# Kernel tuning notes

Measured on AMD Instinct MI355X. Metric: run time of the kernel, lower is better.

The kernel has to match this reference:

```python
import jax, jax.numpy as jnp
import numpy as np
import math

B, C, H, W = 4, 256, 56, 56
RC = 32  # max(256 // 8, 8)
EPS = 1e-5


def _conv(x, w, pad):
    return jax.lax.conv_general_dilated(
        x, w, window_strides=(1, 1), padding=[(pad, pad), (pad, pad)],
        dimension_numbers=('NCHW', 'OIHW', 'NCHW'))


def setup_inputs() -> dict:
    key = jax.random.key(0)
    ks = jax.random.split(key, 9)
    s = 0.05  # keep attention logits in a sane range
    return {
        'x': jax.random.normal(ks[0], (B, C, H, W), jnp.float32),
        'wq1': jax.random.normal(ks[1], (RC, C, 1, 1), jnp.float32) * s,
        'wq3': jax.random.normal(ks[2], (RC, C, 3, 3), jnp.float32) * s,
        'wq5': jax.random.normal(ks[3], (RC, C, 5, 5), jnp.float32) * s,
        'wq7': jax.random.normal(ks[4], (RC, C, 7, 7), jnp.float32) * s,
        'wk': jax.random.normal(ks[5], (RC, C, 1, 1), jnp.float32) * s,
        'wv': jax.random.normal(ks[6], (C, C, 1, 1), jnp.float32) * s,
        'wproj': jax.random.normal(ks[7], (C, 4 * C, 1, 1), jnp.float32) * s,
        'gamma': jnp.ones((C,), jnp.float32),
        'beta': jnp.zeros((C,), jnp.float32),
    }


def reference(x, wq1, wq3, wq5, wq7, wk, wv, wproj, gamma, beta):
    b, c, h, w = x.shape
    hw = h * w
    scale = 1.0 / math.sqrt(RC)
    k = _conv(x, wk, 0).reshape(b, RC, hw)   # [B, RC, HW]
    v = _conv(x, wv, 0).reshape(b, c, hw)    # [B, C, HW]
    attended = []
    for wq, pad in ((wq1, 0), (wq3, 1), (wq5, 2), (wq7, 3)):
        q = _conv(x, wq, pad).reshape(b, RC, hw)          # [B, RC, HW]
        scores = jnp.einsum('bri,brj->bij', q, k) * scale  # [B, HW, HW]
        attn = jax.nn.softmax(scores, axis=-1)
        att = jnp.einsum('bcj,bij->bci', v, attn)          # [B, C, HW]
        attended.append(att.reshape(b, c, h, w))
    concat = jnp.concatenate(attended, axis=1)             # [B, 4C, H, W]
    out = _conv(concat, wproj, 0) + x                      # residual before BN
    # BatchNorm2d in training mode: batch stats (biased var), affine
    mean = out.mean(axis=(0, 2, 3), keepdims=True)
    var = out.var(axis=(0, 2, 3), keepdims=True)
    out = (out - mean) * jax.lax.rsqrt(var + EPS)
    return out * gamma[None, :, None, None] + beta[None, :, None, None]
```

## Files before the change

kernel.cpp:

```cpp
#include <hip/hip_runtime.h>
#include <hip/hip_bf16.h>
#include <math.h>

#define HW 3136
#define WIDTH 56
#define CC 256
#define BB 4
#define RCH 32
#define NJT (HW / 64)
#define TSPLIT 25
#define SCLOG2E 0.2550437041556575f

using bf16x8 = __attribute__((ext_vector_type(8))) short;
using f32x4  = __attribute__((ext_vector_type(4))) float;

static __device__ __forceinline__ unsigned short f2bf(float f) {
    __hip_bfloat16 h = __float2bfloat16(f);
    return *reinterpret_cast<unsigned short*>(&h);
}

__global__ __launch_bounds__(256) void prep_weights(
    const float* __restrict__ wq3, const float* __restrict__ wq5,
    const float* __restrict__ wq7, const float* __restrict__ wproj,
    const float* __restrict__ wk, const float* __restrict__ wq1,
    const float* __restrict__ wv,
    unsigned short* __restrict__ Wb3, unsigned short* __restrict__ Wb5,
    unsigned short* __restrict__ Wb7, unsigned short* __restrict__ Wpb,
    unsigned short* __restrict__ Wkq, unsigned short* __restrict__ Wvb) {
    int e = blockIdx.x * 256 + threadIdx.x;
    if (e < 73728) {
        int c = e & 255, r = (e >> 8) & 31, t = e >> 13;
        Wb3[e] = f2bf(wq3[((size_t)r * 256 + c) * 9 + t]);
    } else if (e < 278528) {
        int i = e - 73728;
        int c = i & 255, r = (i >> 8) & 31, t = i >> 13;
        Wb5[i] = f2bf(wq5[((size_t)r * 256 + c) * 25 + t]);
    } else if (e < 679936) {
        int i = e - 278528;
        int c = i & 255, r = (i >> 8) & 31, t = i >> 13;
        Wb7[i] = f2bf(wq7[((size_t)r * 256 + c) * 49 + t]);
    } else if (e < 942080) {
        int i = e - 679936;
        Wpb[i] = f2bf(wproj[i]);
    } else if (e < 958464) {
        int i = e - 942080;
        Wkq[i] = f2bf(i < 8192 ? wk[i] : wq1[i - 8192]);
    } else if (e < 1024000) {
        int i = e - 958464;
        Wvb[i] = f2bf(wv[i]);
    }
}

__global__ __launch_bounds__(256) void transpose_x(
    const float* __restrict__ x, unsigned short* __restrict__ xT) {
    __shared__ unsigned short tile[32][33];
    const int b = blockIdx.z;
    const int i0 = blockIdx.x * 32, c0 = blockIdx.y * 32;
    const int tx = threadIdx.x & 31, ty = threadIdx.x >> 5;
    #pragma unroll
    for (int k = 0; k < 4; ++k)
        tile[ty + k * 8][tx] = f2bf(x[((size_t)b * CC + c0 + ty + k * 8) * HW + i0 + tx]);
    __syncthreads();
    #pragma unroll
    for (int k = 0; k < 4; ++k)
        xT[((size_t)b * HW + i0 + ty + k * 8) * 256 + c0 + tx] = tile[tx][ty + k * 8];
}

__global__ __launch_bounds__(256) void qk32_mfma(
    const unsigned short* __restrict__ xT, const unsigned short* __restrict__ Wkq,
    unsigned short* __restrict__ Kt, unsigned short* __restrict__ Qt) {
    const int b = blockIdx.y, z = blockIdx.z;
    const int i0 = blockIdx.x * 64;
    const int t = threadIdx.x;
    const int lane = t & 63, w = t >> 6, lg = lane >> 4, li = lane & 15;

    unsigned short* outp = z == 0 ? Kt : Qt;
    const float osc = z == 0 ? 1.0f : SCLOG2E;
    const unsigned short* wb = Wkq + z * 8192;
    const unsigned short* xb = xT + ((size_t)b * HW + i0 + w * 16 + li) * 256;

    const f32x4 z4 = (f32x4){0.f, 0.f, 0.f, 0.f};
    f32x4 acc[2] = {z4, z4};

    for (int c0 = 0; c0 < 256; c0 += 32) {
        bf16x8 ax = *(const bf16x8*)(xb + c0 + lg * 8);
        #pragma unroll
        for (int rs = 0; rs < 2; ++rs) {
            bf16x8 bw = *(const bf16x8*)(wb + (size_t)(rs * 16 + li) * 256 + c0 + lg * 8);
            acc[rs] = __builtin_amdgcn_mfma_f32_16x16x32_bf16(ax, bw, acc[rs], 0, 0, 0);
        }
    }
    unsigned short* qb = outp + ((size_t)b * HW + i0 + w * 16 + lg * 4) * 32;
    #pragma unroll
    for (int rs = 0; rs < 2; ++rs)
        #pragma unroll
        for (int r = 0; r < 4; ++r)
            qb[(size_t)r * 32 + rs * 16 + li] = f2bf(acc[rs][r] * osc);
}

__global__ __launch_bounds__(256) void v_mfma(
    const unsigned short* __restrict__ xT, const unsigned short* __restrict__ Wvb,
    unsigned short* __restrict__ Vb) {
    const int b = blockIdx.y;
    const int i0 = blockIdx.x * 32;
    const int t = threadIdx.x;
    const int lane = t & 63, w = t >> 6, lg = lane >> 4, li = lane & 15;

    const f32x4 z4 = (f32x4){0.f, 0.f, 0.f, 0.f};
    f32x4 acc[4][2];
    #pragma unroll
    for (int ct = 0; ct < 4; ++ct) { acc[ct][0] = z4; acc[ct][1] = z4; }

    const unsigned short* xb = xT + (size_t)b * HW * 256;

    for (int c0 = 0; c0 < 256; c0 += 32) {
        bf16x8 bx[2];
        #pragma unroll
        for (int is = 0; is < 2; ++is)
            bx[is] = *(const bf16x8*)(xb + (size_t)(i0 + is * 16 + li) * 256 + c0 + lg * 8);
        #pragma unroll
        for (int ct = 0; ct < 4; ++ct) {
            bf16x8 aw = *(const bf16x8*)(
                Wvb + (size_t)(w * 64 + ct * 16 + li) * 256 + c0 + lg * 8);
            #pragma unroll
            for (int is = 0; is < 2; ++is)
                acc[ct][is] = __builtin_amdgcn_mfma_f32_16x16x32_bf16(
                    aw, bx[is], acc[ct][is], 0, 0, 0);
        }
    }
    #pragma unroll
    for (int ct = 0; ct < 4; ++ct)
        #pragma unroll
        for (int is = 0; is < 2; ++is)
            #pragma unroll
            for (int r = 0; r < 4; ++r)
                Vb[((size_t)b * CC + w * 64 + ct * 16 + lg * 4 + r) * HW +
                   i0 + is * 16 + li] = f2bf(acc[ct][is][r]);
}

template <int KS>
static __device__ __forceinline__ void qconv_body(
    const unsigned short* __restrict__ xT,
    const unsigned short* __restrict__ Wb,
    unsigned short* __restrict__ q,
    unsigned short (*xs)[40]) {
    constexpr int P = (KS - 1) / 2;
    constexpr int KT = KS * KS;
    constexpr int ROWS = 64 + 114 * P;
    const int b = blockIdx.y;
    const int i0 = blockIdx.x * 64;
    const int t = threadIdx.x;
    const int lane = t & 63;
    const int w = t >> 6;
    const int li = lane & 15;
    const int lg = lane >> 4;

    const int base = i0 - P * 57;
    const int mycol = (i0 + w * 16 + li) % WIDTH;

    f32x4 acc[2];
    acc[0] = (f32x4){0.f, 0.f, 0.f, 0.f};
    acc[1] = (f32x4){0.f, 0.f, 0.f, 0.f};

    const unsigned short* xTb = xT + (size_t)b * HW * 256;

    for (int c0 = 0; c0 < 256; c0 += 32) {
        __syncthreads();
        for (int e = t; e < ROWS * 4; e += 256) {
            int row = e >> 2, cs = e & 3;
            int gidx = base + row;
            uint4 val = make_uint4(0, 0, 0, 0);
            if (gidx >= 0 && gidx < HW)
                val = *(const uint4*)(xTb + (size_t)gidx * 256 + c0 + cs * 8);
            *(uint4*)(&xs[row][cs * 8]) = val;
        }
        __syncthreads();

        #pragma unroll
        for (int tap = 0; tap < KT; ++tap) {
            const int dx = tap % KS - P;
            const int poff = (tap / KS) * WIDTH + tap % KS;
            bf16x8 a = *(const bf16x8*)(&xs[w * 16 + li + poff][lg * 8]);
            if ((unsigned)(mycol + dx) >= (unsigned)WIDTH)
                a = (bf16x8){0, 0, 0, 0, 0, 0, 0, 0};
            const unsigned short* wrow =
                Wb + (size_t)tap * 32 * 256 + c0 + lg * 8;
            bf16x8 b0 = *(const bf16x8*)(wrow + (size_t)li * 256);
            bf16x8 b1 = *(const bf16x8*)(wrow + (size_t)(16 + li) * 256);
            acc[0] = __builtin_amdgcn_mfma_f32_16x16x32_bf16(a, b0, acc[0], 0, 0, 0);
            acc[1] = __builtin_amdgcn_mfma_f32_16x16x32_bf16(a, b1, acc[1], 0, 0, 0);
        }
    }

    unsigned short* qb = q + ((size_t)b * HW + i0 + w * 16 + lg * 4) * 32;
    #pragma unroll
    for (int rs = 0; rs < 2; ++rs)
        #pragma unroll
        for (int r = 0; r < 4; ++r)
            qb[(size_t)r * 32 + rs * 16 + li] = f2bf(acc[rs][r] * SCLOG2E);
}

__global__ __launch_bounds__(256) void qconv_all(
    const unsigned short* __restrict__ xT,
    const unsigned short* __restrict__ Wb3,
    const unsigned short* __restrict__ Wb5,
    const unsigned short* __restrict__ Wb7,
    unsigned short* __restrict__ Qt) {
    __shared__ unsigned short xs[406][40];
    const size_t QSLICE = (size_t)BB * HW * 32;
    if (blockIdx.z == 0)      qconv_body<3>(xT, Wb3, Qt + 1 * QSLICE, xs);
    else if (blockIdx.z == 1) qconv_body<5>(xT, Wb5, Qt + 2 * QSLICE, xs);
    else                      qconv_body<7>(xT, Wb7, Qt + 3 * QSLICE, xs);
}

__global__ __launch_bounds__(256) void flashmfma(
    const unsigned short* __restrict__ Qt, const unsigned short* __restrict__ Kt,
    const unsigned short* __restrict__ Vb, unsigned short* __restrict__ P0,
    unsigned short* __restrict__ P1, float* __restrict__ Lsum) {
    const int F = blockIdx.x;
    const int xcd = F & 7;
    const int within = F >> 3;
    const int q4 = within / 49;
    const int i0 = (within % 49) * 64;
    const int pair = xcd + 8 * (q4 & 1);
    const int split = q4 >> 1;
    const int b = pair & 3;
    const int g = pair >> 2;

    const int t = threadIdx.x;
    const int lane = t & 63;
    const int w = t >> 6;
    const int lg = lane >> 4;
    const int li = lane & 15;

    __shared__ __align__(16) unsigned short Ps[64][72];

    const bf16x8 aq = *(const bf16x8*)(
        Qt + ((size_t)(g * BB + b) * HW + i0 + w * 16 + li) * 32 + lg * 8);

    const f32x4 z4 = (f32x4){0.f, 0.f, 0.f, 0.f};
    f32x4 acc[4][4];
    #pragma unroll
    for (int ct = 0; ct < 4; ++ct)
        #pragma unroll
        for (int is = 0; is < 4; ++is) acc[ct][is] = z4;

    float lsum[4] = {0.f, 0.f, 0.f, 0.f};

    const unsigned short* Kb = Kt + (size_t)b * HW * 32;
    const unsigned short* Vw = Vb + ((size_t)b * CC + w * 64) * HW;

    const int jt0 = split == 0 ? 0 : TSPLIT;
    const int jt1 = split == 0 ? TSPLIT : NJT;

    for (int jt = jt0; jt < jt1; ++jt) {
        const int j0 = jt * 64;

        bf16x8 vf[4][2];
        #pragma unroll
        for (int ct = 0; ct < 4; ++ct) {
            vf[ct][0] = *(const bf16x8*)(
                Vw + (size_t)(ct * 16 + li) * HW + j0 + lg * 8);
            vf[ct][1] = *(const bf16x8*)(
                Vw + (size_t)(ct * 16 + li) * HW + j0 + 32 + lg * 8);
        }

        f32x4 S[4];
        #pragma unroll
        for (int j2 = 0; j2 < 4; ++j2) {
            bf16x8 bk = *(const bf16x8*)(Kb + (size_t)(j0 + j2 * 16 + li) * 32 + lg * 8);
            S[j2] = __builtin_amdgcn_mfma_f32_16x16x32_bf16(aq, bk, z4, 0, 0, 0);
        }

        unsigned int pk0[4], pk1[4];
        #pragma unroll
        for (int r = 0; r < 4; ++r) {
            float p0 = __builtin_amdgcn_exp2f(S[0][r]);
            float p1 = __builtin_amdgcn_exp2f(S[1][r]);
            float p2 = __builtin_amdgcn_exp2f(S[2][r]);
            float p3 = __builtin_amdgcn_exp2f(S[3][r]);
            lsum[r] += (p0 + p1) + (p2 + p3);
            asm("v_cvt_pk_bf16_f32 %0, %1, %2" : "=v"(pk0[r]) : "v"(p0), "v"(p1));
            asm("v_cvt_pk_bf16_f32 %0, %1, %2" : "=v"(pk1[r]) : "v"(p2), "v"(p3));
        }

        __syncthreads();
        #pragma unroll
        for (int r = 0; r < 4; ++r) {
            const int row = w * 16 + lg * 4 + r;
            Ps[row][li]      = (unsigned short)pk0[r];
            Ps[row][16 + li] = (unsigned short)(pk0[r] >> 16);
            Ps[row][32 + li] = (unsigned short)pk1[r];
            Ps[row][48 + li] = (unsigned short)(pk1[r] >> 16);
        }
        __syncthreads();

        bf16x8 bp[4][2];
        #pragma unroll
        for (int is = 0; is < 4; ++is)
            #pragma unroll
            for (int ks = 0; ks < 2; ++ks)
                bp[is][ks] = *(const bf16x8*)(&Ps[is * 16 + li][ks * 32 + lg * 8]);

        __builtin_amdgcn_s_setprio(1);
        #pragma unroll
        for (int ct = 0; ct < 4; ++ct) {
            #pragma unroll
            for (int is = 0; is < 4; ++is) {
                acc[ct][is] = __builtin_amdgcn_mfma_f32_16x16x32_bf16(
                    vf[ct][0], bp[is][0], acc[ct][is], 0, 0, 0);
                acc[ct][is] = __builtin_amdgcn_mfma_f32_16x16x32_bf16(
                    vf[ct][1], bp[is][1], acc[ct][is], 0, 0, 0);
            }
        }
        __builtin_amdgcn_s_setprio(0);
    }

    #pragma unroll
    for (int r = 0; r < 4; ++r) {
        float s = lsum[r];
        #pragma unroll
        for (int off = 1; off < 16; off <<= 1) s += __shfl_xor(s, off);
        if (li == 0)
            Lsum[(size_t)split * 16 * HW + (size_t)(g * BB + b) * HW +
                 i0 + w * 16 + lg * 4 + r] = s;
    }

    unsigned short* Pp = split == 0 ? P0 : P1;
    #pragma unroll
    for (int ct = 0; ct < 4; ++ct)
        #pragma unroll
        for (int is = 0; is < 4; ++is) {
            unsigned int lo, hi;
            asm("v_cvt_pk_bf16_f32 %0, %1, %2"
                : "=v"(lo) : "v"(acc[ct][is][0]), "v"(acc[ct][is][1]));
            asm("v_cvt_pk_bf16_f32 %0, %1, %2"
                : "=v"(hi) : "v"(acc[ct][is][2]), "v"(acc[ct][is][3]));
            uint2 pk; pk.x = lo; pk.y = hi;
            *(uint2*)(Pp + ((size_t)b * HW + i0 + is * 16 + li) * 1024 +
                      g * 256 + w * 64 + ct * 16 + lg * 4) = pk;
        }
}

__global__ __launch_bounds__(256) void combine_att(
    unsigned short* __restrict__ Pio, const unsigned short* __restrict__ P1,
    const float* __restrict__ Lsum) {
    const int b = blockIdx.y;
    const int hw = blockIdx.x * 2 + (threadIdx.x >> 7);
    const int lp = threadIdx.x & 127;
    const int c0 = lp * 8;
    const int g = c0 >> 8;

    const size_t lidx = (size_t)(g * BB + b) * HW + hw;
    const float invl = 1.f / (Lsum[lidx] + Lsum[(size_t)16 * HW + lidx]);

    const size_t off = ((size_t)b * HW + hw) * 1024 + c0;
    uint4 ua = *(const uint4*)(Pio + off);
    uint4 ub = *(const uint4*)(P1 + off);
    unsigned int a[4] = {ua.x, ua.y, ua.z, ua.w};
    unsigned int bb[4] = {ub.x, ub.y, ub.z, ub.w};
    unsigned int o[4];
    #pragma unroll
    for (int k = 0; k < 4; ++k) {
        float a0 = __uint_as_float(a[k] << 16);
        float a1 = __uint_as_float(a[k] & 0xffff0000u);
        float b0 = __uint_as_float(bb[k] << 16);
        float b1 = __uint_as_float(bb[k] & 0xffff0000u);
        float f0 = (a0 + b0) * invl;
        float f1 = (a1 + b1) * invl;
        asm("v_cvt_pk_bf16_f32 %0, %1, %2" : "=v"(o[k]) : "v"(f0), "v"(f1));
    }
    uint4 uo; uo.x = o[0]; uo.y = o[1]; uo.z = o[2]; uo.w = o[3];
    *(uint4*)(Pio + off) = uo;
}

__global__ __launch_bounds__(256) void gemm_proj(
    const unsigned short* __restrict__ ATTt, const unsigned short* __restrict__ Wpb,
    const float* __restrict__ x, float* __restrict__ out) {
    const int b = blockIdx.y;
    const int i0 = blockIdx.x * 32;
    const int t = threadIdx.x;
    const int lane = t & 63;
    const int w = t >> 6;
    const int lg = lane >> 4;
    const int li = lane & 15;

    const f32x4 z4 = (f32x4){0.f, 0.f, 0.f, 0.f};
    f32x4 acc[4][2];
    #pragma unroll
    for (int ct = 0; ct < 4; ++ct) { acc[ct][0] = z4; acc[ct][1] = z4; }

    const unsigned short* ab = ATTt + (size_t)b * HW * 1024;

    for (int k0 = 0; k0 < 1024; k0 += 32) {
        bf16x8 afr[2];
        #pragma unroll
        for (int is = 0; is < 2; ++is)
            afr[is] = *(const bf16x8*)(
                ab + (size_t)(i0 + is * 16 + li) * 1024 + k0 + lg * 8);
        #pragma unroll
        for (int ct = 0; ct < 4; ++ct) {
            bf16x8 wf = *(const bf16x8*)(
                Wpb + (size_t)(w * 64 + ct * 16 + li) * 1024 + k0 + lg * 8);
            #pragma unroll
            for (int is = 0; is < 2; ++is)
                acc[ct][is] = __builtin_amdgcn_mfma_f32_16x16x32_bf16(
                    wf, afr[is], acc[ct][is], 0, 0, 0);
        }
    }

    #pragma unroll
    for (int ct = 0; ct < 4; ++ct)
        #pragma unroll
        for (int is = 0; is < 2; ++is)
            #pragma unroll
            for (int r = 0; r < 4; ++r) {
                int co = w * 64 + ct * 16 + lg * 4 + r;
                size_t o = ((size_t)b * CC + co) * HW + i0 + is * 16 + li;
                out[o] = acc[ct][is][r] + x[o];
            }
}

__global__ __launch_bounds__(256) void bnstats(
    const float* __restrict__ out, float* __restrict__ mean,
    float* __restrict__ rstd) {
    const int c = blockIdx.x;
    float s = 0.f, s2 = 0.f;
    for (int e = threadIdx.x; e < BB * HW; e += 256) {
        int b = e / HW, i = e - b * HW;
        float v = out[((size_t)b * CC + c) * HW + i];
        s += v; s2 += v * v;
    }
    __shared__ float rs[256], rs2[256];
    rs[threadIdx.x] = s; rs2[threadIdx.x] = s2;
    __syncthreads();
    for (int st = 128; st > 0; st >>= 1) {
        if (threadIdx.x < st) {
            rs[threadIdx.x] += rs[threadIdx.x + st];
            rs2[threadIdx.x] += rs2[threadIdx.x + st];
        }
        __syncthreads();
    }
    if (threadIdx.x == 0) {
        const float n = (float)(BB * HW);
        float m = rs[0] / n;
        float var = rs2[0] / n - m * m;
        mean[c] = m;
        rstd[c] = rsqrtf(var + 1e-5f);
    }
}

__global__ __launch_bounds__(256) void bnapply(
    float* __restrict__ out, const float* __restrict__ mean,
    const float* __restrict__ rstd, const float* __restrict__ gamma,
    const float* __restrict__ beta) {
    size_t idx = (size_t)blockIdx.x * 256 + threadIdx.x;
    if (idx < (size_t)BB * CC * HW) {
        int c = (int)((idx / HW) % CC);
        out[idx] = (out[idx] - mean[c]) * rstd[c] * gamma[c] + beta[c];
    }
}

extern "C" void kernel_launch(void* const* d_in, const int* in_sizes, int n_in,
                              void* d_out, int out_size, void* d_ws, size_t ws_size,
                              hipStream_t stream) {
    const float* x     = (const float*)d_in[0];
    const float* wq1   = (const float*)d_in[1];
    const float* wq3   = (const float*)d_in[2];
    const float* wq5   = (const float*)d_in[3];
    const float* wq7   = (const float*)d_in[4];
    const float* wk    = (const float*)d_in[5];
    const float* wv    = (const float*)d_in[6];
    const float* wproj = (const float*)d_in[7];
    const float* gamma = (const float*)d_in[8];
    const float* beta  = (const float*)d_in[9];
    float* out = (float*)d_out;

    unsigned short* P0   = (unsigned short*)d_ws;
    unsigned short* P1   = P0 + (size_t)BB * HW * 1024;
    float* Lsum          = (float*)(P1 + (size_t)BB * HW * 1024);
    unsigned short* Kt   = (unsigned short*)(Lsum + (size_t)2 * 16 * HW);
    unsigned short* Qt   = Kt + (size_t)BB * HW * 32;
    unsigned short* Vb   = Qt + (size_t)4 * BB * HW * 32;
    unsigned short* xT   = Vb + (size_t)BB * CC * HW;
    unsigned short* Wb3  = xT + (size_t)BB * HW * CC;
    unsigned short* Wb5  = Wb3 + (size_t)9 * 32 * 256;
    unsigned short* Wb7  = Wb5 + (size_t)25 * 32 * 256;
    unsigned short* Wpb  = Wb7 + (size_t)49 * 32 * 256;
    unsigned short* Wkq  = Wpb + (size_t)256 * 1024;
    unsigned short* Wvb  = Wkq + (size_t)2 * 32 * 256;
    float* mean = (float*)(Wvb + (size_t)256 * 256);
    float* rstd = mean + CC;

    dim3 blk(256);

    prep_weights<<<dim3(4000), blk, 0, stream>>>(
        wq3, wq5, wq7, wproj, wk, wq1, wv, Wb3, Wb5, Wb7, Wpb, Wkq, Wvb);
    transpose_x<<<dim3(HW / 32, CC / 32, BB), blk, 0, stream>>>(x, xT);

    qk32_mfma<<<dim3(HW / 64, BB, 2), blk, 0, stream>>>(xT, Wkq, Kt, Qt);
    v_mfma<<<dim3(HW / 32, BB), blk, 0, stream>>>(xT, Wvb, Vb);

    qconv_all<<<dim3(HW / 64, BB, 3), blk, 0, stream>>>(xT, Wb3, Wb5, Wb7, Qt);

    flashmfma<<<dim3(8 * 4 * (HW / 64)), blk, 0, stream>>>(Qt, Kt, Vb, P0, P1, Lsum);
    combine_att<<<dim3(HW / 2, BB), blk, 0, stream>>>(P0, P1, Lsum);

    gemm_proj<<<dim3(HW / 32, BB), blk, 0, stream>>>(P0, Wpb, x, out);

    bnstats<<<dim3(CC), blk, 0, stream>>>(out, mean, rstd);
    bnapply<<<dim3((BB * CC * HW + 255) / 256), blk, 0, stream>>>(out, mean, rstd, gamma, beta);
}
```

Before: 486.0 us.

## Fuse split-softmax combine into projection GEMM and merge 3x3/5x5 q-convs

Result: no change. 485.9 us (-0.0%).

```diff
diff --git a/kernel.cpp b/kernel.cpp
--- a/kernel.cpp
+++ b/kernel.cpp
@@ -200,6 +200,83 @@
             qb[(size_t)r * 32 + rs * 16 + li] = f2bf(acc[rs][r] * SCLOG2E);
 }
 
+static __device__ __forceinline__ void qconv35_body(
+    const unsigned short* __restrict__ xT,
+    const unsigned short* __restrict__ Wb3,
+    const unsigned short* __restrict__ Wb5,
+    unsigned short* __restrict__ q3, unsigned short* __restrict__ q5,
+    unsigned short (*xs)[40]) {
+    constexpr int P = 2;
+    constexpr int ROWS = 64 + 114 * P;
+    const int b = blockIdx.y;
+    const int i0 = blockIdx.x * 64;
+    const int t = threadIdx.x;
+    const int lane = t & 63;
+    const int w = t >> 6;
+    const int li = lane & 15;
+    const int lg = lane >> 4;
+
+    const int base = i0 - P * 57;
+    const int mycol = (i0 + w * 16 + li) % WIDTH;
+
+    const f32x4 z4 = (f32x4){0.f, 0.f, 0.f, 0.f};
+    f32x4 acc3[2] = {z4, z4}, acc5[2] = {z4, z4};
+
+    const unsigned short* xTb = xT + (size_t)b * HW * 256;
+
+    for (int c0 = 0; c0 < 256; c0 += 32) {
+        __syncthreads();
+        for (int e = t; e < ROWS * 4; e += 256) {
+            int row = e >> 2, cs = e & 3;
+            int gidx = base + row;
+            uint4 val = make_uint4(0, 0, 0, 0);
+            if (gidx >= 0 && gidx < HW)
+                val = *(const uint4*)(xTb + (size_t)gidx * 256 + c0 + cs * 8);
+            *(uint4*)(&xs[row][cs * 8]) = val;
+        }
+        __syncthreads();
+
+        #pragma unroll
+        for (int dy = -2; dy <= 2; ++dy) {
+            #pragma unroll
+            for (int dx = -2; dx <= 2; ++dx) {
+                const int poff = (dy + 2) * WIDTH + (dx + 2);
+                bf16x8 a = *(const bf16x8*)(&xs[w * 16 + li + poff][lg * 8]);
+                if ((unsigned)(mycol + dx) >= (unsigned)WIDTH)
+                    a = (bf16x8){0, 0, 0, 0, 0, 0, 0, 0};
+                {
+                    const int t5 = (dy + 2) * 5 + (dx + 2);
+                    const unsigned short* wrow =
+                        Wb5 + (size_t)t5 * 32 * 256 + c0 + lg * 8;
+                    bf16x8 b0 = *(const bf16x8*)(wrow + (size_t)li * 256);
+                    bf16x8 b1 = *(const bf16x8*)(wrow + (size_t)(16 + li) * 256);
+                    acc5[0] = __builtin_amdgcn_mfma_f32_16x16x32_bf16(a, b0, acc5[0], 0, 0, 0);
+                    acc5[1] = __builtin_amdgcn_mfma_f32_16x16x32_bf16(a, b1, acc5[1], 0, 0, 0);
+                }
+                if (dy >= -1 && dy <= 1 && dx >= -1 && dx <= 1) {
+                    const int t3 = (dy + 1) * 3 + (dx + 1);
+                    const unsigned short* wrow =
+                        Wb3 + (size_t)t3 * 32 * 256 + c0 + lg * 8;
+                    bf16x8 b0 = *(const bf16x8*)(wrow + (size_t)li * 256);
+                    bf16x8 b1 = *(const bf16x8*)(wrow + (size_t)(16 + li) * 256);
+                    acc3[0] = __builtin_amdgcn_mfma_f32_16x16x32_bf16(a, b0, acc3[0], 0, 0, 0);
+                    acc3[1] = __builtin_amdgcn_mfma_f32_16x16x32_bf16(a, b1, acc3[1], 0, 0, 0);
+                }
+            }
+        }
+    }
+
+    unsigned short* qb3 = q3 + ((size_t)b * HW + i0 + w * 16 + lg * 4) * 32;
+    unsigned short* qb5 = q5 + ((size_t)b * HW + i0 + w * 16 + lg * 4) * 32;
+    #pragma unroll
+    for (int rs = 0; rs < 2; ++rs)
+        #pragma unroll
+        for (int r = 0; r < 4; ++r) {
+            qb3[(size_t)r * 32 + rs * 16 + li] = f2bf(acc3[rs][r] * SCLOG2E);
+            qb5[(size_t)r * 32 + rs * 16 + li] = f2bf(acc5[rs][r] * SCLOG2E);
+        }
+}
+
 __global__ __launch_bounds__(256) void qconv_all(
     const unsigned short* __restrict__ xT,
     const unsigned short* __restrict__ Wb3,
@@ -208,9 +285,10 @@
     unsigned short* __restrict__ Qt) {
     __shared__ unsigned short xs[406][40];
     const size_t QSLICE = (size_t)BB * HW * 32;
-    if (blockIdx.z == 0)      qconv_body<3>(xT, Wb3, Qt + 1 * QSLICE, xs);
-    else if (blockIdx.z == 1) qconv_body<5>(xT, Wb5, Qt + 2 * QSLICE, xs);
-    else                      qconv_body<7>(xT, Wb7, Qt + 3 * QSLICE, xs);
+    if (blockIdx.z == 0)
+        qconv_body<7>(xT, Wb7, Qt + 3 * QSLICE, xs);
+    else
+        qconv35_body(xT, Wb3, Wb5, Qt + 1 * QSLICE, Qt + 2 * QSLICE, xs);
 }
 
 __global__ __launch_bounds__(256) void flashmfma(
@@ -342,40 +420,9 @@
         }
 }
 
-__global__ __launch_bounds__(256) void combine_att(
-    unsigned short* __restrict__ Pio, const unsigned short* __restrict__ P1,
-    const float* __restrict__ Lsum) {
-    const int b = blockIdx.y;
-    const int hw = blockIdx.x * 2 + (threadIdx.x >> 7);
-    const int lp = threadIdx.x & 127;
-    const int c0 = lp * 8;
-    const int g = c0 >> 8;
-
-    const size_t lidx = (size_t)(g * BB + b) * HW + hw;
-    const float invl = 1.f / (Lsum[lidx] + Lsum[(size_t)16 * HW + lidx]);
-
-    const size_t off = ((size_t)b * HW + hw) * 1024 + c0;
-    uint4 ua = *(const uint4*)(Pio + off);
-    uint4 ub = *(const uint4*)(P1 + off);
-    unsigned int a[4] = {ua.x, ua.y, ua.z, ua.w};
-    unsigned int bb[4] = {ub.x, ub.y, ub.z, ub.w};
-    unsigned int o[4];
-    #pragma unroll
-    for (int k = 0; k < 4; ++k) {
-        float a0 = __uint_as_float(a[k] << 16);
-        float a1 = __uint_as_float(a[k] & 0xffff0000u);
-        float b0 = __uint_as_float(bb[k] << 16);
-        float b1 = __uint_as_float(bb[k] & 0xffff0000u);
-        float f0 = (a0 + b0) * invl;
-        float f1 = (a1 + b1) * invl;
-        asm("v_cvt_pk_bf16_f32 %0, %1, %2" : "=v"(o[k]) : "v"(f0), "v"(f1));
-    }
-    uint4 uo; uo.x = o[0]; uo.y = o[1]; uo.z = o[2]; uo.w = o[3];
-    *(uint4*)(Pio + off) = uo;
-}
-
 __global__ __launch_bounds__(256) void gemm_proj(
-    const unsigned short* __restrict__ ATTt, const unsigned short* __restrict__ Wpb,
+    const unsigned short* __restrict__ P0, const unsigned short* __restrict__ P1,
+    const unsigned short* __restrict__ Wpb, const float* __restrict__ Lsum,
     const float* __restrict__ x, float* __restrict__ out) {
     const int b = blockIdx.y;
     const int i0 = blockIdx.x * 32;
@@ -386,27 +433,55 @@
     const int li = lane & 15;
 
     const f32x4 z4 = (f32x4){0.f, 0.f, 0.f, 0.f};
-    f32x4 acc[4][2];
-    #pragma unroll
-    for (int ct = 0; ct < 4; ++ct) { acc[ct][0] = z4; acc[ct][1] = z4; }
-
-    const unsigned short* ab = ATTt + (size_t)b * HW * 1024;
-
-    for (int k0 = 0; k0 < 1024; k0 += 32) {
-        bf16x8 afr[2];
-        #pragma unroll
-        for (int is = 0; is < 2; ++is)
-            afr[is] = *(const bf16x8*)(
-                ab + (size_t)(i0 + is * 16 + li) * 1024 + k0 + lg * 8);
-        #pragma unroll
-        for (int ct = 0; ct < 4; ++ct) {
-            bf16x8 wf = *(const bf16x8*)(
-                Wpb + (size_t)(w * 64 + ct * 16 + li) * 1024 + k0 + lg * 8);
+    f32x4 fin[4][2];
+    #pragma unroll
+    for (int ct = 0; ct < 4; ++ct) { fin[ct][0] = z4; fin[ct][1] = z4; }
+
+    const unsigned short* a0 = P0 + (size_t)b * HW * 1024;
+    const unsigned short* a1 = P1 + (size_t)b * HW * 1024;
+
+    for (int g = 0; g < 4; ++g) {
+        float invl[2];
+        #pragma unroll
+        for (int is = 0; is < 2; ++is) {
+            size_t lidx = (size_t)(g * BB + b) * HW + i0 + is * 16 + li;
+            invl[is] = 1.f / (Lsum[lidx] + Lsum[(size_t)16 * HW + lidx]);
+        }
+
+        f32x4 acc[4][2];
+        #pragma unroll
+        for (int ct = 0; ct < 4; ++ct) { acc[ct][0] = z4; acc[ct][1] = z4; }
+
+        for (int k0 = g * 256; k0 < (g + 1) * 256; k0 += 32) {
+            bf16x8 afr0[2], afr1[2];
+            #pragma unroll
+            for (int is = 0; is < 2; ++is) {
+                afr0[is] = *(const bf16x8*)(
+                    a0 + (size_t)(i0 + is * 16 + li) * 1024 + k0 + lg * 8);
+                afr1[is] = *(const bf16x8*)(
+                    a1 + (size_t)(i0 + is * 16 + li) * 1024 + k0 + lg * 8);
+            }
+            #pragma unroll
+            for (int ct = 0; ct < 4; ++ct) {
+                bf16x8 wf = *(const bf16x8*)(
+                    Wpb + (size_t)(w * 64 + ct * 16 + li) * 1024 + k0 + lg * 8);
+                #pragma unroll
+                for (int is = 0; is < 2; ++is) {
+                    acc[ct][is] = __builtin_amdgcn_mfma_f32_16x16x32_bf16(
+                        wf, afr0[is], acc[ct][is], 0, 0, 0);
+                    acc[ct][is] = __builtin_amdgcn_mfma_f32_16x16x32_bf16(
+                        wf, afr1[is], acc[ct][is], 0, 0, 0);
+                }
+            }
+        }
+
+        #pragma unroll
+        for (int ct = 0; ct < 4; ++ct)
             #pragma unroll
             for (int is = 0; is < 2; ++is)
-                acc[ct][is] = __builtin_amdgcn_mfma_f32_16x16x32_bf16(
-                    wf, afr[is], acc[ct][is], 0, 0, 0);
-        }
+                #pragma unroll
+                for (int r = 0; r < 4; ++r)
+                    fin[ct][is][r] += acc[ct][is][r] * invl[is];
     }
 
     #pragma unroll
@@ -417,7 +492,7 @@
             for (int r = 0; r < 4; ++r) {
                 int co = w * 64 + ct * 16 + lg * 4 + r;
                 size_t o = ((size_t)b * CC + co) * HW + i0 + is * 16 + li;
-                out[o] = acc[ct][is][r] + x[o];
+                out[o] = fin[ct][is][r] + x[o];
             }
 }
 
@@ -501,12 +576,11 @@
     qk32_mfma<<<dim3(HW / 64, BB, 2), blk, 0, stream>>>(xT, Wkq, Kt, Qt);
     v_mfma<<<dim3(HW / 32, BB), blk, 0, stream>>>(xT, Wvb, Vb);
 
-    qconv_all<<<dim3(HW / 64, BB, 3), blk, 0, stream>>>(xT, Wb3, Wb5, Wb7, Qt);
+    qconv_all<<<dim3(HW / 64, BB, 2), blk, 0, stream>>>(xT, Wb3, Wb5, Wb7, Qt);
 
     flashmfma<<<dim3(8 * 4 * (HW / 64)), blk, 0, stream>>>(Qt, Kt, Vb, P0, P1, Lsum);
-    combine_att<<<dim3(HW / 2, BB), blk, 0, stream>>>(P0, P1, Lsum);
-
-    gemm_proj<<<dim3(HW / 32, BB), blk, 0, stream>>>(P0, Wpb, x, out);
+
+    gemm_proj<<<dim3(HW / 32, BB), blk, 0, stream>>>(P0, P1, Wpb, Lsum, x, out);
 
     bnstats<<<dim3(CC), blk, 0, stream>>>(out, mean, rstd);
     bnapply<<<dim3((BB * CC * HW + 255) / 256), blk, 0, stream>>>(out, mean, rstd, gamma, beta);
```
